# Kernel optimization log

Measured on AMD Instinct MI355X. Metric: run time of the kernel, lower is better.

The kernel has to match this reference:

```python
import jax, jax.numpy as jnp
import numpy as np

B, T, L, C = 512, 512, 48, 128
BLANK = C - 1          # Keras ctc_batch_cost uses last class as blank
EPS = 1e-7             # K.epsilon() added before log, as in ctc_batch_cost
NEG = -1e30            # finite 'log zero' (avoids NaN in gradients)


def setup_inputs() -> dict:
    key = jax.random.key(0)
    k1, k2 = jax.random.split(key)
    logits = jax.random.normal(k1, (B, T, C), dtype=jnp.float32)
    y_pred = jax.nn.softmax(logits, axis=-1)  # ctc_batch_cost expects probabilities
    y_true = jax.random.randint(k2, (B, L), 0, C - 1, dtype=jnp.int32)  # labels in [0, C-2]
    return {"y_true": y_true, "y_pred": y_pred}


def ctc_loss(y_true, y_pred):
    # Faithful jax version of K.ctc_batch_cost with full input/label lengths
    # (the layer passes input_length=T, label_length=L for every sample).
    Bn, Tn, Cn = y_pred.shape
    Ln = y_true.shape[1]
    S = 2 * Ln + 1  # extended label: blank,l0,blank,l1,...,blank

    log_probs = jnp.log(y_pred + EPS)  # [B,T,C]

    # Extended label sequence [B,S]
    ext = jnp.full((Bn, S), BLANK, dtype=jnp.int32).at[:, 1::2].set(y_true)
    # Gather per-step log-probs of extended labels: [B,T,S]
    lp_ext = jnp.take_along_axis(log_probs, ext[:, None, :], axis=2)

    # Skip transition s-2 -> s allowed iff ext[s] != blank and ext[s] != ext[s-2]
    ext_m2 = jnp.pad(ext[:, :-2], ((0, 0), (2, 0)), constant_values=BLANK)
    allow2 = (ext != BLANK) & (ext != ext_m2)  # [B,S]

    neg = jnp.float32(NEG)
    alpha0 = (jnp.full((Bn, S), neg)
              .at[:, 0].set(lp_ext[:, 0, 0])
              .at[:, 1].set(lp_ext[:, 0, 1]))

    pad1 = jnp.full((Bn, 1), neg)
    pad2 = jnp.full((Bn, 2), neg)

    def step(alpha, lp_t):
        a1 = jnp.concatenate([pad1, alpha[:, :-1]], axis=1)
        a2 = jnp.concatenate([pad2, alpha[:, :-2]], axis=1)
        a2 = jnp.where(allow2, a2, neg)
        new = jnp.logaddexp(jnp.logaddexp(alpha, a1), a2) + lp_t
        return new, None

    lp_seq = jnp.swapaxes(lp_ext, 0, 1)[1:]  # [T-1,B,S]
    alphaT, _ = jax.lax.scan(step, alpha0, lp_seq)

    ll = jnp.logaddexp(alphaT[:, S - 1], alphaT[:, S - 2])  # [B]
    return -ll[:, None]  # [B,1], matching ctc_batch_cost output shape


def reference(y_true, y_pred):
    return ctc_loss(y_true, y_pred)
```

## Files before the change

### kernel.cpp

```cpp
#include <hip/hip_runtime.h>
#include <stdint.h>

#define Bn 512
#define Tn 512
#define Ln 48
#define Cn 128
#define BLANKC 127
#define EPSf 1e-7f
#define LN2f 0.6931471805599453f

template<int CTRL>
__device__ __forceinline__ float dpp_f0(float x) {
    int r = __builtin_amdgcn_update_dpp(0, __float_as_int(x), CTRL, 0xF, 0xF, true);
    return __int_as_float(r);
}
template<int CTRL>
__device__ __forceinline__ int dpp_i_keep(int x) {
    return __builtin_amdgcn_update_dpp(x, x, CTRL, 0xF, 0xF, false);
}

__global__ void __launch_bounds__(128, 1) ctc_fwd(
        const int* __restrict__ yt,
        const float* __restrict__ yp,
        float* __restrict__ out)
{
    const int b = blockIdx.x;
    const int w = threadIdx.x >> 6;
    const int l = threadIdx.x & 63;

    __shared__ float ring[2][8192];
    __shared__ float xb0[64], xb1[64];
    __shared__ int   xEb[64];
    __shared__ int   rmax[4];
    __shared__ float rsum[4];

    const bool lab_ok = (l < Ln);
    int  cls1 = BLANKC;
    bool allow2 = false;
    if (lab_ok) {
        cls1 = yt[b * Ln + l];
        if (l >= 1) allow2 = (cls1 != yt[b * Ln + l - 1]);
    }

    float a0, a1;
    int   E = 0;
    float* lds = &ring[w][0];
    const float* gbase = yp + (size_t)b * (Tn * Cn);

#define STAGE(FIRSTROW, SLOTBASE)                                            \
    {                                                                        \
        const float* gr_ = gbase + (size_t)(FIRSTROW) * Cn + (l << 2);       \
        _Pragma("unroll")                                                    \
        for (int j = 0; j < 8; ++j)                                          \
            __builtin_amdgcn_global_load_lds(                                \
                (const __attribute__((address_space(1))) uint32_t*)(gr_ + j * 256), \
                (__attribute__((address_space(3))) uint32_t*)&lds[(SLOTBASE) + j * 256], \
                16, 0, 0);                                                   \
    }

#define WAIT8() asm volatile("s_waitcnt vmcnt(8)" ::: "memory");
#define WAIT0() asm volatile("s_waitcnt vmcnt(0)" ::: "memory");

#define RENORM()                                                     \
    {                                                                \
        float m_ = fmaxf(a0, a1);                                    \
        int   e_ = ((__float_as_int(m_) >> 23) & 0xFF) - 126;        \
        float sc_ = __int_as_float((127 - e_) << 23);                \
        a0 *= sc_; a1 *= sc_;                                        \
        E += e_;                                                     \
    }

    if (w == 0) {
        STAGE(0, 0) STAGE(16, 2048) STAGE(32, 4096)
        WAIT8()

        a0 = (l == 0) ? lds[127]  + EPSf : 0.0f;
        a1 = (l == 0) ? lds[cls1] + EPSf : 0.0f;

        float pb1 = lds[(1 << 7) + 127], pl1 = lds[(1 << 7) + cls1];
        float pb2 = lds[(2 << 7) + 127], pl2 = lds[(2 << 7) + cls1];
        float pb3 = lds[(3 << 7) + 127], pl3 = lds[(3 << 7) + cls1];
        float pb0 = lds[(4 << 7) + 127], pl0 = lds[(4 << 7) + cls1];

#define FSTEP(PB, PL, LID, dopf)                                     \
    {                                                                \
        float nb_ = 0.0f, nl_ = 0.0f;                                \
        if (dopf) { nb_ = lds[(LID) + 127];                          \
                    nl_ = lds[(LID) + cls1]; }                       \
        float p0 = (PB) + EPSf;                                      \
        float p1 = lab_ok ? (PL) + EPSf : 0.0f;                      \
        float h1 = dpp_f0<0x138>(a1);                                \
        int   Eh = dpp_i_keep<0x138>(E);                             \
        int   d_ = Eh - E;                                           \
        int   shA = min(-d_, 0);                                     \
        int   shH = min(d_, 0);                                      \
        E = max(E, Eh);                                              \
        float a0c = ldexpf(a0, shA);                                 \
        float a1c = ldexpf(a1, shA);                                 \
        float h1c = ldexpf(h1, shH);                                 \
        float t0 = a0c + h1c;                                        \
        float u  = a1c + (allow2 ? t0 : a0c);                        \
        a0 = t0 * p0;                                                \
        a1 = u * p1;                                                 \
        if (dopf) { (PB) = nb_; (PL) = nl_; }                        \
    }

        FSTEP(pb1, pl1, (5 << 7), true)
        FSTEP(pb2, pl2, (6 << 7), true)
        FSTEP(pb3, pl3, (7 << 7), true)
        RENORM()
        FSTEP(pb0, pl0, (8 << 7), true)
        FSTEP(pb1, pl1, (9 << 7), true)
        FSTEP(pb2, pl2, (10 << 7), true)
        FSTEP(pb3, pl3, (11 << 7), true)
        RENORM()
        FSTEP(pb0, pl0, (12 << 7), true)
        FSTEP(pb1, pl1, (13 << 7), true)
        FSTEP(pb2, pl2, (14 << 7), true)
        FSTEP(pb3, pl3, (15 << 7), true)
        RENORM()
        FSTEP(pb0, pl0, 2048 + (0 << 7), true)
        FSTEP(pb1, pl1, 2048 + (1 << 7), true)
        FSTEP(pb2, pl2, 2048 + (2 << 7), true)
        FSTEP(pb3, pl3, 2048 + (3 << 7), true)
        RENORM()
        STAGE(48, 6144) WAIT8()

#define F16(IB, INX)                                                 \
        FSTEP(pb0, pl0, (IB) + (4 << 7), true)                       \
        FSTEP(pb1, pl1, (IB) + (5 << 7), true)                       \
        FSTEP(pb2, pl2, (IB) + (6 << 7), true)                       \
        FSTEP(pb3, pl3, (IB) + (7 << 7), true)                       \
        RENORM()                                                     \
        FSTEP(pb0, pl0, (IB) + (8 << 7), true)                       \
        FSTEP(pb1, pl1, (IB) + (9 << 7), true)                       \
        FSTEP(pb2, pl2, (IB) + (10 << 7), true)                      \
        FSTEP(pb3, pl3, (IB) + (11 << 7), true)                      \
        RENORM()                                                     \
        FSTEP(pb0, pl0, (IB) + (12 << 7), true)                      \
        FSTEP(pb1, pl1, (IB) + (13 << 7), true)                      \
        FSTEP(pb2, pl2, (IB) + (14 << 7), true)                      \
        FSTEP(pb3, pl3, (IB) + (15 << 7), true)                      \
        RENORM()                                                     \
        FSTEP(pb0, pl0, (INX) + (0 << 7), true)                      \
        FSTEP(pb1, pl1, (INX) + (1 << 7), true)                      \
        FSTEP(pb2, pl2, (INX) + (2 << 7), true)                      \
        FSTEP(pb3, pl3, (INX) + (3 << 7), true)                      \
        RENORM()

        for (int c = 1; c <= 12; ++c) {
            const int ib  = (c & 3) << 11;
            const int inx = ((c + 1) & 3) << 11;
            F16(ib, inx)
            STAGE((c + 3) * 16, ((c + 3) & 3) << 11)
            WAIT8()
        }
        F16(1 << 11, 2 << 11)
        WAIT0()
        F16(2 << 11, 3 << 11)
        {
            const int ib = 3 << 11;
            FSTEP(pb0, pl0, ib + (4 << 7), true)
            FSTEP(pb1, pl1, ib + (5 << 7), true)
            FSTEP(pb2, pl2, ib + (6 << 7), true)
            FSTEP(pb3, pl3, ib + (7 << 7), true)
            RENORM()
            FSTEP(pb0, pl0, ib + (8 << 7), true)
            FSTEP(pb1, pl1, ib + (9 << 7), true)
            FSTEP(pb2, pl2, ib + (10 << 7), true)
            FSTEP(pb3, pl3, ib + (11 << 7), true)
            RENORM()
            FSTEP(pb0, pl0, ib + (12 << 7), true)
            FSTEP(pb1, pl1, ib + (13 << 7), true)
            FSTEP(pb2, pl2, ib + (14 << 7), true)
            FSTEP(pb3, pl3, ib + (15 << 7), true)
            RENORM()
            FSTEP(pb0, pl0, 0, false)
            FSTEP(pb1, pl1, 0, false)
            FSTEP(pb2, pl2, 0, false)
            FSTEP(pb3, pl3, 0, false)
            RENORM()
        }
#undef FSTEP
#undef F16
    } else {
        STAGE(496, 0) STAGE(480, 2048) STAGE(464, 4096)
        WAIT8()

        a0 = (l == 48) ? 1.0f : 0.0f;
        a1 = (l == 47) ? 1.0f : 0.0f;

        float pb0 = lds[(15 << 7) + 127], pl0 = lds[(15 << 7) + cls1];
        float pb1 = lds[(14 << 7) + 127], pl1 = lds[(14 << 7) + cls1];
        float pb2 = lds[(13 << 7) + 127], pl2 = lds[(13 << 7) + cls1];
        float pb3 = lds[(12 << 7) + 127], pl3 = lds[(12 << 7) + cls1];

#define BSTEP(PB, PL, LID, dopf)                                     \
    {                                                                \
        float nb_ = 0.0f, nl_ = 0.0f;                                \
        if (dopf) { nb_ = lds[(LID) + 127];                          \
                    nl_ = lds[(LID) + cls1]; }                       \
        float p0 = (PB) + EPSf;                                      \
        float p1 = lab_ok ? (PL) + EPSf : 0.0f;                      \
        float g0 = a0 * p0;                                          \
        float g1 = a1 * p1;                                          \
        float w_ = allow2 ? g1 : 0.0f;                               \
        float g0u = dpp_f0<0x130>(g0);                               \
        float wu  = dpp_f0<0x130>(w_);                               \
        int   Eh = dpp_i_keep<0x130>(E);                             \
        int   d_ = Eh - E;                                           \
        int   shA = min(-d_, 0);                                     \
        int   shH = min(d_, 0);                                      \
        E = max(E, Eh);                                              \
        float up = g0u + wu;                                         \
        a0 = ldexpf(g0 + g1, shA);                                   \
        a1 = ldexpf(g1, shA) + ldexpf(up, shH);                      \
        if (dopf) { (PB) = nb_; (PL) = nl_; }                        \
    }

#define B16(IB, INX)                                                 \
        BSTEP(pb0, pl0, (IB) + (11 << 7), true)                      \
        BSTEP(pb1, pl1, (IB) + (10 << 7), true)                      \
        BSTEP(pb2, pl2, (IB) + (9 << 7), true)                       \
        BSTEP(pb3, pl3, (IB) + (8 << 7), true)                       \
        RENORM()                                                     \
        BSTEP(pb0, pl0, (IB) + (7 << 7), true)                       \
        BSTEP(pb1, pl1, (IB) + (6 << 7), true)                       \
        BSTEP(pb2, pl2, (IB) + (5 << 7), true)                       \
        BSTEP(pb3, pl3, (IB) + (4 << 7), true)                       \
        RENORM()                                                     \
        BSTEP(pb0, pl0, (IB) + (3 << 7), true)                       \
        BSTEP(pb1, pl1, (IB) + (2 << 7), true)                       \
        BSTEP(pb2, pl2, (IB) + (1 << 7), true)                       \
        BSTEP(pb3, pl3, (IB) + (0 << 7), true)                       \
        RENORM()                                                     \
        BSTEP(pb0, pl0, (INX) + (15 << 7), true)                     \
        BSTEP(pb1, pl1, (INX) + (14 << 7), true)                     \
        BSTEP(pb2, pl2, (INX) + (13 << 7), true)                     \
        BSTEP(pb3, pl3, (INX) + (12 << 7), true)                     \
        RENORM()

        B16(0, 1 << 11)
        STAGE(448, 6144) WAIT8()

        for (int c = 1; c <= 12; ++c) {
            const int ib  = (c & 3) << 11;
            const int inx = ((c + 1) & 3) << 11;
            B16(ib, inx)
            STAGE(496 - 16 * (c + 3), ((c + 3) & 3) << 11)
            WAIT8()
        }
        B16(1 << 11, 2 << 11)
        WAIT0()
        B16(2 << 11, 3 << 11)
        {
            const int ib = 3 << 11;
            BSTEP(pb0, pl0, ib + (11 << 7), true)
            BSTEP(pb1, pl1, ib + (10 << 7), true)
            BSTEP(pb2, pl2, ib + (9 << 7), true)
            BSTEP(pb3, pl3, ib + (8 << 7), true)
            RENORM()
            BSTEP(pb0, pl0, ib + (7 << 7), true)
            BSTEP(pb1, pl1, ib + (6 << 7), true)
            BSTEP(pb2, pl2, ib + (5 << 7), true)
            BSTEP(pb3, pl3, ib + (4 << 7), true)
            RENORM()
            BSTEP(pb0, pl0, ib + (3 << 7), true)
            BSTEP(pb1, pl1, ib + (2 << 7), true)
            BSTEP(pb2, pl2, ib + (1 << 7), true)
            BSTEP(pb3, pl3, ib + (0 << 7), true)
            RENORM()
            BSTEP(pb0, pl0, 0, false)
            BSTEP(pb1, pl1, 0, false)
            BSTEP(pb2, pl2, 0, false)
            BSTEP(pb3, pl3, 0, false)
            RENORM()
        }
#undef BSTEP
#undef B16

        xb0[l] = a0; xb1[l] = a1; xEb[l] = E;
    }

    __syncthreads();

    if (w == 0) {
        float B0 = xb0[l], B1 = xb1[l];
        int   EB = xEb[l];
        float c  = a0 * B0 + a1 * B1;
        int   Ec = (c == 0.0f) ? (int)0xC0000000 : (E + EB);
        int m = Ec;
        m = max(m, dpp_i_keep<0x111>(m));
        m = max(m, dpp_i_keep<0x112>(m));
        m = max(m, dpp_i_keep<0x114>(m));
        m = max(m, dpp_i_keep<0x118>(m));
        if ((l & 15) == 15) rmax[l >> 4] = m;
        int Emax = max(max(rmax[0], rmax[1]), max(rmax[2], rmax[3]));
        float v = ldexpf(c, Ec - Emax);
        v += dpp_f0<0x111>(v);
        v += dpp_f0<0x112>(v);
        v += dpp_f0<0x114>(v);
        v += dpp_f0<0x118>(v);
        if ((l & 15) == 15) rsum[l >> 4] = v;
        if (l == 0) {
            float sum = rsum[0] + rsum[1] + rsum[2] + rsum[3];
            out[b] = -LN2f * (__log2f(sum) + (float)Emax);
        }
    }
#undef STAGE
#undef WAIT8
#undef WAIT0
#undef RENORM
}

extern "C" void kernel_launch(void* const* d_in, const int* in_sizes, int n_in,
                              void* d_out, int out_size, void* d_ws, size_t ws_size,
                              hipStream_t stream) {
    const int*   yt  = (const int*)d_in[0];
    const float* yp  = (const float*)d_in[1];
    float*       out = (float*)d_out;
    hipLaunchKernelGGL(ctc_fwd, dim3(Bn), dim3(128), 0, stream, yt, yp, out);
}
```

Before: 27.67 us.

## Switch CTC alpha/beta recursion to fp64 with a shared wave-wide exponent

Carries the forward and backward probability recursions in double precision with one exponent per wavefront instead of one per lane. This drops the per-step exponent exchange and ldexp alignment, and renormalizes only once every 16 steps using a cross-lane max of the high words. The final combination becomes a plain fp64 sum with no max-align pass. The cost is fp64 multiply/add throughput and two DPP moves per 64-bit shift, plus LDS round trips inside each renorm. Lanes far below the wave maximum may also lose precision.

```diff
diff --git a/kernel.cpp b/kernel.cpp
--- a/kernel.cpp
+++ b/kernel.cpp
@@ -6,7 +6,7 @@
 #define Ln 48
 #define Cn 128
 #define BLANKC 127
-#define EPSf 1e-7f
+#define EPSd 1e-7
 #define LN2f 0.6931471805599453f
 
 template<int CTRL>
@@ -17,6 +17,15 @@
 template<int CTRL>
 __device__ __forceinline__ int dpp_i_keep(int x) {
     return __builtin_amdgcn_update_dpp(x, x, CTRL, 0xF, 0xF, false);
+}
+template<int CTRL>
+__device__ __forceinline__ double dpp64_f0(double x) {
+    long long v = __double_as_longlong(x);
+    int lo = (int)(v & 0xffffffffLL);
+    int hi = (int)(v >> 32);
+    lo = __builtin_amdgcn_update_dpp(0, lo, CTRL, 0xF, 0xF, true);
+    hi = __builtin_amdgcn_update_dpp(0, hi, CTRL, 0xF, 0xF, true);
+    return __longlong_as_double(((long long)(unsigned int)lo) | ((long long)hi << 32));
 }
 
 __global__ void __launch_bounds__(128, 1) ctc_fwd(
@@ -28,11 +37,11 @@
     const int w = threadIdx.x >> 6;
     const int l = threadIdx.x & 63;
 
-    __shared__ float ring[2][8192];
-    __shared__ float xb0[64], xb1[64];
-    __shared__ int   xEb[64];
-    __shared__ int   rmax[4];
-    __shared__ float rsum[4];
+    __shared__ float  ring[2][8192];
+    __shared__ double xb0d[64], xb1d[64];
+    __shared__ int    xEbs;
+    __shared__ int    rnmax[2][4];
+    __shared__ double rsumd[4];
 
     const bool lab_ok = (l < Ln);
     int  cls1 = BLANKC;
@@ -42,8 +51,8 @@
         if (l >= 1) allow2 = (cls1 != yt[b * Ln + l - 1]);
     }
 
-    float a0, a1;
-    int   E = 0;
+    double a0, a1;
+    int    E = 0;
     float* lds = &ring[w][0];
     const float* gbase = yp + (size_t)b * (Tn * Cn);
 
@@ -61,11 +70,20 @@
 #define WAIT8() asm volatile("s_waitcnt vmcnt(8)" ::: "memory");
 #define WAIT0() asm volatile("s_waitcnt vmcnt(0)" ::: "memory");
 
-#define RENORM()                                                     \
+#define RENORM64()                                                   \
     {                                                                \
-        float m_ = fmaxf(a0, a1);                                    \
-        int   e_ = ((__float_as_int(m_) >> 23) & 0xFF) - 126;        \
-        float sc_ = __int_as_float((127 - e_) << 23);                \
+        int h0_ = (int)(__double_as_longlong(a0) >> 32);             \
+        int h1_ = (int)(__double_as_longlong(a1) >> 32);             \
+        int mh_ = max(h0_, h1_);                                     \
+        mh_ = max(mh_, dpp_i_keep<0x111>(mh_));                      \
+        mh_ = max(mh_, dpp_i_keep<0x112>(mh_));                      \
+        mh_ = max(mh_, dpp_i_keep<0x114>(mh_));                      \
+        mh_ = max(mh_, dpp_i_keep<0x118>(mh_));                      \
+        if ((l & 15) == 15) rnmax[w][l >> 4] = mh_;                  \
+        int g_ = max(max(rnmax[w][0], rnmax[w][1]),                  \
+                     max(rnmax[w][2], rnmax[w][3]));                 \
+        int e_ = ((g_ >> 20) & 0x7FF) - 1022;                        \
+        double sc_ = __longlong_as_double((long long)(1023 - e_) << 52); \
         a0 *= sc_; a1 *= sc_;                                        \
         E += e_;                                                     \
     }
@@ -74,8 +92,8 @@
         STAGE(0, 0) STAGE(16, 2048) STAGE(32, 4096)
         WAIT8()
 
-        a0 = (l == 0) ? lds[127]  + EPSf : 0.0f;
-        a1 = (l == 0) ? lds[cls1] + EPSf : 0.0f;
+        a0 = (l == 0) ? (double)lds[127]  + EPSd : 0.0;
+        a1 = (l == 0) ? (double)lds[cls1] + EPSd : 0.0;
 
         float pb1 = lds[(1 << 7) + 127], pl1 = lds[(1 << 7) + cls1];
         float pb2 = lds[(2 << 7) + 127], pl2 = lds[(2 << 7) + cls1];
@@ -87,19 +105,11 @@
         float nb_ = 0.0f, nl_ = 0.0f;                                \
         if (dopf) { nb_ = lds[(LID) + 127];                          \
                     nl_ = lds[(LID) + cls1]; }                       \
-        float p0 = (PB) + EPSf;                                      \
-        float p1 = lab_ok ? (PL) + EPSf : 0.0f;                      \
-        float h1 = dpp_f0<0x138>(a1);                                \
-        int   Eh = dpp_i_keep<0x138>(E);                             \
-        int   d_ = Eh - E;                                           \
-        int   shA = min(-d_, 0);                                     \
-        int   shH = min(d_, 0);                                      \
-        E = max(E, Eh);                                              \
-        float a0c = ldexpf(a0, shA);                                 \
-        float a1c = ldexpf(a1, shA);                                 \
-        float h1c = ldexpf(h1, shH);                                 \
-        float t0 = a0c + h1c;                                        \
-        float u  = a1c + (allow2 ? t0 : a0c);                        \
+        double p0 = (double)(PB) + EPSd;                             \
+        double p1 = lab_ok ? (double)(PL) + EPSd : 0.0;              \
+        double h1 = dpp64_f0<0x138>(a1);                             \
+        double t0 = a0 + h1;                                         \
+        double u  = a1 + (allow2 ? t0 : a0);                         \
         a0 = t0 * p0;                                                \
         a1 = u * p1;                                                 \
         if (dopf) { (PB) = nb_; (PL) = nl_; }                        \
@@ -108,22 +118,19 @@
         FSTEP(pb1, pl1, (5 << 7), true)
         FSTEP(pb2, pl2, (6 << 7), true)
         FSTEP(pb3, pl3, (7 << 7), true)
-        RENORM()
         FSTEP(pb0, pl0, (8 << 7), true)
         FSTEP(pb1, pl1, (9 << 7), true)
         FSTEP(pb2, pl2, (10 << 7), true)
         FSTEP(pb3, pl3, (11 << 7), true)
-        RENORM()
         FSTEP(pb0, pl0, (12 << 7), true)
         FSTEP(pb1, pl1, (13 << 7), true)
         FSTEP(pb2, pl2, (14 << 7), true)
         FSTEP(pb3, pl3, (15 << 7), true)
-        RENORM()
         FSTEP(pb0, pl0, 2048 + (0 << 7), true)
         FSTEP(pb1, pl1, 2048 + (1 << 7), true)
         FSTEP(pb2, pl2, 2048 + (2 << 7), true)
         FSTEP(pb3, pl3, 2048 + (3 << 7), true)
-        RENORM()
+        RENORM64()
         STAGE(48, 6144) WAIT8()
 
 #define F16(IB, INX)                                                 \
@@ -131,22 +138,19 @@
         FSTEP(pb1, pl1, (IB) + (5 << 7), true)                       \
         FSTEP(pb2, pl2, (IB) + (6 << 7), true)                       \
         FSTEP(pb3, pl3, (IB) + (7 << 7), true)                       \
-        RENORM()                                                     \
         FSTEP(pb0, pl0, (IB) + (8 << 7), true)                       \
         FSTEP(pb1, pl1, (IB) + (9 << 7), true)                       \
         FSTEP(pb2, pl2, (IB) + (10 << 7), true)                      \
         FSTEP(pb3, pl3, (IB) + (11 << 7), true)                      \
-        RENORM()                                                     \
         FSTEP(pb0, pl0, (IB) + (12 << 7), true)                      \
         FSTEP(pb1, pl1, (IB) + (13 << 7), true)                      \
         FSTEP(pb2, pl2, (IB) + (14 << 7), true)                      \
         FSTEP(pb3, pl3, (IB) + (15 << 7), true)                      \
-        RENORM()                                                     \
         FSTEP(pb0, pl0, (INX) + (0 << 7), true)                      \
         FSTEP(pb1, pl1, (INX) + (1 << 7), true)                      \
         FSTEP(pb2, pl2, (INX) + (2 << 7), true)                      \
         FSTEP(pb3, pl3, (INX) + (3 << 7), true)                      \
-        RENORM()
+        RENORM64()
 
         for (int c = 1; c <= 12; ++c) {
             const int ib  = (c & 3) << 11;
@@ -164,22 +168,19 @@
             FSTEP(pb1, pl1, ib + (5 << 7), true)
             FSTEP(pb2, pl2, ib + (6 << 7), true)
             FSTEP(pb3, pl3, ib + (7 << 7), true)
-            RENORM()
             FSTEP(pb0, pl0, ib + (8 << 7), true)
             FSTEP(pb1, pl1, ib + (9 << 7), true)
             FSTEP(pb2, pl2, ib + (10 << 7), true)
             FSTEP(pb3, pl3, ib + (11 << 7), true)
-            RENORM()
             FSTEP(pb0, pl0, ib + (12 << 7), true)
             FSTEP(pb1, pl1, ib + (13 << 7), true)
             FSTEP(pb2, pl2, ib + (14 << 7), true)
             FSTEP(pb3, pl3, ib + (15 << 7), true)
-            RENORM()
             FSTEP(pb0, pl0, 0, false)
             FSTEP(pb1, pl1, 0, false)
             FSTEP(pb2, pl2, 0, false)
             FSTEP(pb3, pl3, 0, false)
-            RENORM()
+            RENORM64()
         }
 #undef FSTEP
 #undef F16
@@ -187,8 +188,8 @@
         STAGE(496, 0) STAGE(480, 2048) STAGE(464, 4096)
         WAIT8()
 
-        a0 = (l == 48) ? 1.0f : 0.0f;
-        a1 = (l == 47) ? 1.0f : 0.0f;
+        a0 = (l == 48) ? 1.0 : 0.0;
+        a1 = (l == 47) ? 1.0 : 0.0;
 
         float pb0 = lds[(15 << 7) + 127], pl0 = lds[(15 << 7) + cls1];
         float pb1 = lds[(14 << 7) + 127], pl1 = lds[(14 << 7) + cls1];
@@ -200,21 +201,14 @@
         float nb_ = 0.0f, nl_ = 0.0f;                                \
         if (dopf) { nb_ = lds[(LID) + 127];                          \
                     nl_ = lds[(LID) + cls1]; }                       \
-        float p0 = (PB) + EPSf;                                      \
-        float p1 = lab_ok ? (PL) + EPSf : 0.0f;                      \
-        float g0 = a0 * p0;                                          \
-        float g1 = a1 * p1;                                          \
-        float w_ = allow2 ? g1 : 0.0f;                               \
-        float g0u = dpp_f0<0x130>(g0);                               \
-        float wu  = dpp_f0<0x130>(w_);                               \
-        int   Eh = dpp_i_keep<0x130>(E);                             \
-        int   d_ = Eh - E;                                           \
-        int   shA = min(-d_, 0);                                     \
-        int   shH = min(d_, 0);                                      \
-        E = max(E, Eh);                                              \
-        float up = g0u + wu;                                         \
-        a0 = ldexpf(g0 + g1, shA);                                   \
-        a1 = ldexpf(g1, shA) + ldexpf(up, shH);                      \
+        double p0 = (double)(PB) + EPSd;                             \
+        double p1 = lab_ok ? (double)(PL) + EPSd : 0.0;              \
+        double g0 = a0 * p0;                                         \
+        double g1 = a1 * p1;                                         \
+        double pre = g0 + (allow2 ? g1 : 0.0);                       \
+        double up = dpp64_f0<0x130>(pre);                            \
+        a0 = g0 + g1;                                                \
+        a1 = g1 + up;                                                \
         if (dopf) { (PB) = nb_; (PL) = nl_; }                        \
     }
 
@@ -223,22 +217,19 @@
         BSTEP(pb1, pl1, (IB) + (10 << 7), true)                      \
         BSTEP(pb2, pl2, (IB) + (9 << 7), true)                       \
         BSTEP(pb3, pl3, (IB) + (8 << 7), true)                       \
-        RENORM()                                                     \
         BSTEP(pb0, pl0, (IB) + (7 << 7), true)                       \
         BSTEP(pb1, pl1, (IB) + (6 << 7), true)                       \
         BSTEP(pb2, pl2, (IB) + (5 << 7), true)                       \
         BSTEP(pb3, pl3, (IB) + (4 << 7), true)                       \
-        RENORM()                                                     \
         BSTEP(pb0, pl0, (IB) + (3 << 7), true)                       \
         BSTEP(pb1, pl1, (IB) + (2 << 7), true)                       \
         BSTEP(pb2, pl2, (IB) + (1 << 7), true)                       \
         BSTEP(pb3, pl3, (IB) + (0 << 7), true)                       \
-        RENORM()                                                     \
         BSTEP(pb0, pl0, (INX) + (15 << 7), true)                     \
         BSTEP(pb1, pl1, (INX) + (14 << 7), true)                     \
         BSTEP(pb2, pl2, (INX) + (13 << 7), true)                     \
         BSTEP(pb3, pl3, (INX) + (12 << 7), true)                     \
-        RENORM()
+        RENORM64()
 
         B16(0, 1 << 11)
         STAGE(448, 6144) WAIT8()
@@ -259,58 +250,49 @@
             BSTEP(pb1, pl1, ib + (10 << 7), true)
             BSTEP(pb2, pl2, ib + (9 << 7), true)
             BSTEP(pb3, pl3, ib + (8 << 7), true)
-            RENORM()
             BSTEP(pb0, pl0, ib + (7 << 7), true)
             BSTEP(pb1, pl1, ib + (6 << 7), true)
             BSTEP(pb2, pl2, ib + (5 << 7), true)
             BSTEP(pb3, pl3, ib + (4 << 7), true)
-            RENORM()
             BSTEP(pb0, pl0, ib + (3 << 7), true)
             BSTEP(pb1, pl1, ib + (2 << 7), true)
             BSTEP(pb2, pl2, ib + (1 << 7), true)
             BSTEP(pb3, pl3, ib + (0 << 7), true)
-            RENORM()
             BSTEP(pb0, pl0, 0, false)
             BSTEP(pb1, pl1, 0, false)
             BSTEP(pb2, pl2, 0, false)
             BSTEP(pb3, pl3, 0, false)
-            RENORM()
+            RENORM64()
         }
 #undef BSTEP
 #undef B16
 
-        xb0[l] = a0; xb1[l] = a1; xEb[l] = E;
+        xb0d[l] = a0; xb1d[l] = a1;
+        if (l == 0) xEbs = E;
     }
 
     __syncthreads();
 
     if (w == 0) {
-        float B0 = xb0[l], B1 = xb1[l];
-        int   EB = xEb[l];
-        float c  = a0 * B0 + a1 * B1;
-        int   Ec = (c == 0.0f) ? (int)0xC0000000 : (E + EB);
-        int m = Ec;
-        m = max(m, dpp_i_keep<0x111>(m));
-        m = max(m, dpp_i_keep<0x112>(m));
-        m = max(m, dpp_i_keep<0x114>(m));
-        m = max(m, dpp_i_keep<0x118>(m));
-        if ((l & 15) == 15) rmax[l >> 4] = m;
-        int Emax = max(max(rmax[0], rmax[1]), max(rmax[2], rmax[3]));
-        float v = ldexpf(c, Ec - Emax);
-        v += dpp_f0<0x111>(v);
-        v += dpp_f0<0x112>(v);
-        v += dpp_f0<0x114>(v);
-        v += dpp_f0<0x118>(v);
-        if ((l & 15) == 15) rsum[l >> 4] = v;
+        double c = a0 * xb0d[l] + a1 * xb1d[l];
+        c += dpp64_f0<0x111>(c);
+        c += dpp64_f0<0x112>(c);
+        c += dpp64_f0<0x114>(c);
+        c += dpp64_f0<0x118>(c);
+        if ((l & 15) == 15) rsumd[l >> 4] = c;
         if (l == 0) {
-            float sum = rsum[0] + rsum[1] + rsum[2] + rsum[3];
-            out[b] = -LN2f * (__log2f(sum) + (float)Emax);
+            double s = rsumd[0] + rsumd[1] + rsumd[2] + rsumd[3];
+            long long sb = __double_as_longlong(s);
+            int se = (int)((sb >> 52) & 0x7FF) - 1022;
+            double m = __longlong_as_double((sb & 0x800FFFFFFFFFFFFFLL) | (1022LL << 52));
+            float lg = __log2f((float)m) + (float)(se + E + xEbs);
+            out[b] = -LN2f * lg;
         }
     }
 #undef STAGE
 #undef WAIT8
 #undef WAIT0
-#undef RENORM
+#undef RENORM64
 }
 
 extern "C" void kernel_launch(void* const* d_in, const int* in_sizes, int n_in,
```

After: 26.79 us. 1.03x faster.
